# Kernel tuning notes

Hardware: AMD Instinct MI355X
Metric: run time of the kernel (lower is better)

## Reference

```python
import jax, jax.numpy as jnp
import numpy as np

N = 50000      # nodes
E = 625000     # directed edges
F_IN, H1, H2, OUT = 128, 128, 64, 50


def setup_inputs() -> dict:
    key = jax.random.key(0)
    ks = jax.random.split(key, 5)
    x = jax.random.normal(ks[0], (N, F_IN), dtype=jnp.float32)
    edge_index = jax.random.randint(ks[1], (2, E), 0, N, dtype=jnp.int64)
    W1 = jax.random.normal(ks[2], (F_IN, H1), dtype=jnp.float32) * 0.05
    b1 = jnp.zeros((H1,), jnp.float32)
    W2 = jax.random.normal(ks[3], (H1, H2), dtype=jnp.float32) * 0.05
    b2 = jnp.zeros((H2,), jnp.float32)
    Wh = jax.random.normal(ks[4], (H2, OUT), dtype=jnp.float32) * 0.05
    bh = jnp.zeros((OUT,), jnp.float32)
    return {"x": x, "edge_index": edge_index, "W1": W1, "b1": b1,
            "W2": W2, "b2": b2, "Wh": Wh, "bh": bh}


def _gcn_conv(h, W, b, src, dst, dinv, n):
    # h' = D^{-1/2} A_hat D^{-1/2} (h W) + b, A_hat includes self-loops
    h = h @ W                                   # [n, out]
    coef = (dinv[src] * dinv[dst])[:, None]      # [e, 1]
    agg = jax.ops.segment_sum(h[src] * coef, dst, num_segments=n)
    return agg + b


def reference(x, edge_index, W1, b1, W2, b2, Wh, bh):
    n = x.shape[0]
    loops = jnp.arange(n, dtype=edge_index.dtype)
    src = jnp.concatenate([edge_index[0], loops])
    dst = jnp.concatenate([edge_index[1], loops])
    # symmetric GCN normalization: deg over destinations (incl. self-loops)
    deg = jax.ops.segment_sum(jnp.ones(src.shape[0], x.dtype), dst, num_segments=n)
    dinv = jnp.where(deg > 0, jax.lax.rsqrt(deg), 0.0)
    # dropout is a no-op in eval mode (training=False)
    h = _gcn_conv(x, W1, b1, src, dst, dinv, n)
    h = jax.nn.relu(h)
    h = _gcn_conv(h, W2, b2, src, dst, dinv, n)
    h = jax.nn.relu(h)
    return h @ Wh + bh
```

## Files before the change

### kernel.cpp

```cpp
#include <hip/hip_runtime.h>

#define F_IN 128
#define HH1 128
#define HH2 64
#define FOUT 50
#define EB 256
#define NBUCK_MAX 256

typedef __attribute__((ext_vector_type(8))) short short8;
typedef __attribute__((ext_vector_type(4))) short s16x4;
typedef __attribute__((ext_vector_type(4))) float f32x4;

__device__ inline short f2bf(float f) {
    union { float f; unsigned u; } v; v.f = f;
    unsigned r = v.u + 0x7fffu + ((v.u >> 16) & 1u);
    return (short)(r >> 16);
}
__device__ inline float bf2f(short s) {
    union { float f; unsigned u; } v; v.u = ((unsigned)(unsigned short)s) << 16;
    return v.f;
}

__device__ inline int detect64(const unsigned* raw) {
    __shared__ int s_is64;
    if (threadIdx.x == 0) s_is64 = 1;
    __syncthreads();
    if (raw[2 * threadIdx.x + 1] != 0u) atomicAnd(&s_is64, 0);
    __syncthreads();
    return s_is64;
}

__global__ __launch_bounds__(256) void bucket_count(
    const int* __restrict__ raw, int E, int nbuck, int* __restrict__ parthist,
    const float* __restrict__ W1, const float* __restrict__ W2,
    const float* __restrict__ Wh, short* __restrict__ W1t,
    short* __restrict__ W2t, short* __restrict__ Wht) {
    __shared__ int hist[4][NBUCK_MAX];
    const int tid = threadIdx.x;
    const int wv = tid >> 6;
    int is64 = detect64((const unsigned*)raw);
    for (int k = tid; k < 4 * NBUCK_MAX; k += 256) ((int*)hist)[k] = 0;
    __syncthreads();
    const int CH = (E + EB - 1) / EB;
    const int e0 = blockIdx.x * CH, e1 = min(E, e0 + CH);
    for (int e = e0 + tid; e < e1; e += 256) {
        int d = is64 ? raw[2 * (long)E + 2 * e] : raw[E + e];
        atomicAdd(&hist[wv][d >> 8], 1);
    }
    __syncthreads();
    for (int k = tid; k < nbuck; k += 256)
        parthist[blockIdx.x * nbuck + k] =
            hist[0][k] + hist[1][k] + hist[2][k] + hist[3][k];
    const int T1 = HH1 * F_IN, T2 = HH2 * HH1, T3 = 64 * HH2;
    int idx = blockIdx.x * 256 + tid;
    if (idx < T1) {
        int c = idx / F_IN, k = idx - c * F_IN;
        W1t[idx] = f2bf(W1[(long)k * HH1 + c]);
    } else if (idx < T1 + T2) {
        int i = idx - T1;
        int c = i / HH1, k = i - c * HH1;
        W2t[i] = f2bf(W2[(long)k * HH2 + c]);
    } else if (idx < T1 + T2 + T3) {
        int i = idx - T1 - T2;
        int c = i / HH2, k = i - c * HH2;
        Wht[i] = f2bf((c < FOUT) ? Wh[(long)k * FOUT + c] : 0.f);
    }
}

__global__ __launch_bounds__(256) void scan_cols(
    int* __restrict__ parthist, int* __restrict__ totals, int* __restrict__ bbase,
    unsigned* __restrict__ done, int nbuck, int E) {
    const int k = blockIdx.x;
    const int t = threadIdx.x;
    __shared__ int sh[256];
    int v = 0;
    if (k < nbuck) v = parthist[t * nbuck + k];
    sh[t] = v;
    __syncthreads();
    for (int off = 1; off < 256; off <<= 1) {
        int tv = (t >= off) ? sh[t - off] : 0;
        __syncthreads();
        sh[t] += tv;
        __syncthreads();
    }
    if (k < nbuck) parthist[t * nbuck + k] = sh[t] - v;
    if (t == 255) totals[k] = (k < nbuck) ? sh[255] : 0;
    __threadfence();
    __syncthreads();
    __shared__ unsigned s_old;
    if (t == 0) s_old = atomicAdd(done, 1u);
    __syncthreads();
    if (s_old % 256u != 255u) return;
    __threadfence();
    int tv2 = totals[t];
    sh[t] = tv2;
    __syncthreads();
    for (int off = 1; off < 256; off <<= 1) {
        int tt = (t >= off) ? sh[t - off] : 0;
        __syncthreads();
        sh[t] += tt;
        __syncthreads();
    }
    if (t < nbuck) bbase[t] = sh[t] - tv2;
    if (t == 0) bbase[nbuck] = E;
}

__global__ __launch_bounds__(256) void scatter_gemm1(
    const int* __restrict__ raw, int E, int nbuck,
    const int* __restrict__ parthist, const int* __restrict__ bbase,
    int2* __restrict__ tmp,
    const float* __restrict__ x, const short* __restrict__ W1t,
    short* __restrict__ h1, int n) {
    const int tid = threadIdx.x;
    if (blockIdx.x < EB) {
        __shared__ int cur[NBUCK_MAX];
        int is64 = detect64((const unsigned*)raw);
        for (int k = tid; k < nbuck; k += 256)
            cur[k] = bbase[k] + parthist[blockIdx.x * nbuck + k];
        __syncthreads();
        const int CH = (E + EB - 1) / EB;
        const int e0 = blockIdx.x * CH, e1 = min(E, e0 + CH);
        for (int e = e0 + tid; e < e1; e += 256) {
            int s, d;
            if (is64) {
                s = raw[2 * e];
                d = raw[2 * (long)E + 2 * e];
            } else {
                s = raw[e];
                d = raw[E + e];
            }
            int pos = atomicAdd(&cur[d >> 8], 1);
            tmp[pos] = make_int2(s, d);
        }
        return;
    }
    const int bid = blockIdx.x - EB;
    const int wave = tid >> 6;
    const int lane = tid & 63;
    const int l15 = lane & 15;
    const int kg = lane >> 4;
    const int rowbase = bid * 64 + wave * 16;
    const int arow = rowbase + l15;
    constexpr int KS = F_IN / 32;

    short8 af[KS];
    if (arow < n) {
        const float* xr = x + (long)arow * F_IN + kg * 8;
#pragma unroll
        for (int ks = 0; ks < KS; ++ks) {
            float4 f0 = *(const float4*)(xr + ks * 32);
            float4 f1 = *(const float4*)(xr + ks * 32 + 4);
            short8 a;
            a[0] = f2bf(f0.x); a[1] = f2bf(f0.y); a[2] = f2bf(f0.z); a[3] = f2bf(f0.w);
            a[4] = f2bf(f1.x); a[5] = f2bf(f1.y); a[6] = f2bf(f1.z); a[7] = f2bf(f1.w);
            af[ks] = a;
        }
    } else {
#pragma unroll
        for (int ks = 0; ks < KS; ++ks) af[ks] = (short8)0;
    }
    const int crowb = rowbase + kg * 4;
#pragma unroll
    for (int ct = 0; ct < HH1 / 16; ++ct) {
        const int col = ct * 16 + l15;
        const short* wr = W1t + (long)col * F_IN + kg * 8;
        f32x4 acc = {0.f, 0.f, 0.f, 0.f};
#pragma unroll
        for (int ks = 0; ks < KS; ++ks) {
            short8 bfr = *(const short8*)(wr + ks * 32);
            acc = __builtin_amdgcn_mfma_f32_16x16x32_bf16(af[ks], bfr, acc, 0, 0, 0);
        }
#pragma unroll
        for (int j = 0; j < 4; ++j) {
            int r = crowb + j;
            if (r < n) h1[(long)r * HH1 + col] = f2bf(acc[j]);
        }
    }
}

__global__ __launch_bounds__(256) void bucket_finalize(
    const int2* __restrict__ tmp, const int* __restrict__ bbase,
    int* __restrict__ rowptr, float* __restrict__ dinv,
    int* __restrict__ csr_src, int n, int nbuck) {
    __shared__ int deg[256];
    __shared__ int cur[256];
    __shared__ int sh[256];
    const int k = blockIdx.x;
    const int tid = threadIdx.x;
    const int b0 = bbase[k], b1 = bbase[k + 1];
    deg[tid] = 0;
    __syncthreads();
    for (int e = b0 + tid; e < b1; e += 256) atomicAdd(&deg[tmp[e].y & 255], 1);
    __syncthreads();
    int v = deg[tid];
    sh[tid] = v;
    __syncthreads();
    for (int off = 1; off < 256; off <<= 1) {
        int t = (tid >= off) ? sh[tid - off] : 0;
        __syncthreads();
        sh[tid] += t;
        __syncthreads();
    }
    int excl = sh[tid] - v;
    cur[tid] = excl;
    int node = (k << 8) + tid;
    if (node < n) {
        rowptr[node] = b0 + excl;
        dinv[node] = rsqrtf((float)v + 1.0f);
    }
    if (k == 0 && tid == 0) rowptr[n] = bbase[nbuck];
    __syncthreads();
    for (int e = b0 + tid; e < b1; e += 256) {
        int2 sd = tmp[e];
        int p = atomicAdd(&cur[sd.y & 255], 1);
        csr_src[b0 + p] = sd.x;
    }
}

template <int FPL>
__device__ inline void gather1(const short* p0, float c0, float* acc) {
    if constexpr (FPL == 8) {
        short8 v0 = *(const short8*)p0;
#pragma unroll
        for (int j = 0; j < 8; ++j) acc[j] = fmaf(c0, bf2f(v0[j]), acc[j]);
    } else {
        s16x4 v0 = *(const s16x4*)p0;
#pragma unroll
        for (int j = 0; j < 4; ++j) acc[j] = fmaf(c0, bf2f(v0[j]), acc[j]);
    }
}

template <int FW, bool OUT_F32>
__global__ __launch_bounds__(256) void agg_mm(
    const short* __restrict__ h, const int* __restrict__ rowptr,
    const int* __restrict__ csr_src, const float* __restrict__ dinv,
    const float* __restrict__ bias_pre, const short* __restrict__ Wt,
    const float* __restrict__ bias_post, void* __restrict__ Yv, int n,
    int ncreal) {
    constexpr int FPL = FW / 16;
    constexpr int LDW = FW + 8;
    constexpr int KS = FW / 32;
    __shared__ short tile[16][LDW];
    const int tid = threadIdx.x;
    const int grp = tid >> 4;
    const int l16 = tid & 15;
    const int node = blockIdx.x * 16 + grp;

    float acc[FPL];
#pragma unroll
    for (int j = 0; j < FPL; ++j) acc[j] = 0.f;

    if (node < n) {
        const float di = dinv[node];
#pragma unroll
        for (int j = 0; j < FPL; ++j) acc[j] = bias_pre[l16 * FPL + j];
        gather1<FPL>(h + (long)node * FW + l16 * FPL, di * di, acc);
        int e = rowptr[node];
        const int end = rowptr[node + 1];
        for (; e + 3 < end; e += 4) {
            int s0 = csr_src[e];
            int s1 = csr_src[e + 1];
            int s2 = csr_src[e + 2];
            int s3 = csr_src[e + 3];
            const short* p0 = h + (long)s0 * FW + l16 * FPL;
            const short* p1 = h + (long)s1 * FW + l16 * FPL;
            const short* p2 = h + (long)s2 * FW + l16 * FPL;
            const short* p3 = h + (long)s3 * FW + l16 * FPL;
            float c0 = dinv[s0] * di;
            float c1 = dinv[s1] * di;
            float c2 = dinv[s2] * di;
            float c3 = dinv[s3] * di;
            if constexpr (FPL == 8) {
                short8 v0 = *(const short8*)p0;
                short8 v1 = *(const short8*)p1;
                short8 v2 = *(const short8*)p2;
                short8 v3 = *(const short8*)p3;
#pragma unroll
                for (int j = 0; j < 8; ++j) acc[j] = fmaf(c0, bf2f(v0[j]), acc[j]);
#pragma unroll
                for (int j = 0; j < 8; ++j) acc[j] = fmaf(c1, bf2f(v1[j]), acc[j]);
#pragma unroll
                for (int j = 0; j < 8; ++j) acc[j] = fmaf(c2, bf2f(v2[j]), acc[j]);
#pragma unroll
                for (int j = 0; j < 8; ++j) acc[j] = fmaf(c3, bf2f(v3[j]), acc[j]);
            } else {
                s16x4 v0 = *(const s16x4*)p0;
                s16x4 v1 = *(const s16x4*)p1;
                s16x4 v2 = *(const s16x4*)p2;
                s16x4 v3 = *(const s16x4*)p3;
#pragma unroll
                for (int j = 0; j < 4; ++j) acc[j] = fmaf(c0, bf2f(v0[j]), acc[j]);
#pragma unroll
                for (int j = 0; j < 4; ++j) acc[j] = fmaf(c1, bf2f(v1[j]), acc[j]);
#pragma unroll
                for (int j = 0; j < 4; ++j) acc[j] = fmaf(c2, bf2f(v2[j]), acc[j]);
#pragma unroll
                for (int j = 0; j < 4; ++j) acc[j] = fmaf(c3, bf2f(v3[j]), acc[j]);
            }
        }
        for (; e < end; ++e) {
            int s0 = csr_src[e];
            gather1<FPL>(h + (long)s0 * FW + l16 * FPL, dinv[s0] * di, acc);
        }
    }
    if constexpr (FPL == 8) {
        short8 o;
#pragma unroll
        for (int j = 0; j < 8; ++j) o[j] = f2bf(fmaxf(acc[j], 0.f));
        *(short8*)&tile[grp][l16 * 8] = o;
    } else {
        s16x4 o;
#pragma unroll
        for (int j = 0; j < 4; ++j) o[j] = f2bf(fmaxf(acc[j], 0.f));
        *(s16x4*)&tile[grp][l16 * 4] = o;
    }
    __syncthreads();

    const int wave = tid >> 6;
    const int lane = tid & 63;
    const int l15 = lane & 15;
    const int kg = lane >> 4;
    const int col = wave * 16 + l15;
    short8 af[KS];
#pragma unroll
    for (int ks = 0; ks < KS; ++ks)
        af[ks] = *(const short8*)&tile[l15][kg * 8 + ks * 32];
    f32x4 c2 = {0.f, 0.f, 0.f, 0.f};
    const short* wr = Wt + (long)col * FW + kg * 8;
#pragma unroll
    for (int ks = 0; ks < KS; ++ks) {
        short8 bfr = *(const short8*)(wr + ks * 32);
        c2 = __builtin_amdgcn_mfma_f32_16x16x32_bf16(af[ks], bfr, c2, 0, 0, 0);
    }
    const int rb = blockIdx.x * 16 + kg * 4;
    if (OUT_F32) {
        float* Y = (float*)Yv;
#pragma unroll
        for (int j = 0; j < 4; ++j) {
            int g = rb + j;
            if (g < n && col < ncreal)
                Y[(long)g * ncreal + col] = c2[j] + bias_post[col];
        }
    } else {
        short* Y = (short*)Yv;
#pragma unroll
        for (int j = 0; j < 4; ++j) {
            int g = rb + j;
            if (g < n) Y[(long)g * 64 + col] = f2bf(c2[j]);
        }
    }
}

static inline size_t al256(size_t x) { return (x + 255) & ~(size_t)255; }

extern "C" void kernel_launch(void* const* d_in, const int* in_sizes, int n_in,
                              void* d_out, int out_size, void* d_ws, size_t ws_size,
                              hipStream_t stream) {
    const float* x    = (const float*)d_in[0];
    const int*   eraw = (const int*)d_in[1];
    const float* W1   = (const float*)d_in[2];
    const float* b1   = (const float*)d_in[3];
    const float* W2   = (const float*)d_in[4];
    const float* b2   = (const float*)d_in[5];
    const float* Wh   = (const float*)d_in[6];
    const float* bh   = (const float*)d_in[7];
    float* out = (float*)d_out;
    const int n = in_sizes[0] / F_IN;
    const int E = in_sizes[1] / 2;
    const int nbuck = (n + 255) >> 8;

    char* p = (char*)d_ws;
    unsigned* done  = (unsigned*)p; p += 256;
    float* dinv     = (float*)p; p += al256((size_t)n * 4);
    int*   rowptr   = (int*)p;   p += al256((size_t)(n + 1) * 4);
    int*   parthist = (int*)p;   p += al256((size_t)EB * nbuck * 4);
    int*   totals   = (int*)p;   p += al256((size_t)NBUCK_MAX * 4);
    int*   bbase    = (int*)p;   p += al256((size_t)(nbuck + 1) * 4);
    int*   csr_src  = (int*)p;   p += al256((size_t)E * 4);
    short* W1t      = (short*)p; p += al256((size_t)HH1 * F_IN * 2);
    short* W2t      = (short*)p; p += al256((size_t)HH2 * HH1 * 2);
    short* Whtp     = (short*)p; p += al256((size_t)64 * HH2 * 2);
    int2*  tmp      = (int2*)p;  p += al256((size_t)E * 8);
    short* h1       = (short*)p; p += al256((size_t)n * HH1 * 2);
    short* h2       = (short*)p;

    dim3 blk(256);
    bucket_count<<<EB, blk, 0, stream>>>(eraw, E, nbuck, parthist,
                                         W1, W2, Wh, W1t, W2t, Whtp);
    scan_cols<<<NBUCK_MAX, blk, 0, stream>>>(parthist, totals, bbase, done, nbuck, E);
    scatter_gemm1<<<EB + (n + 63) / 64, blk, 0, stream>>>(
        eraw, E, nbuck, parthist, bbase, tmp, x, W1t, h1, n);
    bucket_finalize<<<nbuck, blk, 0, stream>>>(tmp, bbase, rowptr, dinv, csr_src, n, nbuck);

    agg_mm<HH1, false><<<(n + 15) / 16, blk, 0, stream>>>(
        h1, rowptr, csr_src, dinv, b1, W2t, nullptr, h2, n, HH2);
    agg_mm<HH2, true><<<(n + 15) / 16, blk, 0, stream>>>(
        h2, rowptr, csr_src, dinv, b2, Whtp, bh, out, n, FOUT);
}
```

Before: 122.9 us.

## Sort nodes by in-degree within buckets to balance aggregation block work

Measured after the change: 130.7 us. 1.06x slower.

```diff
diff --git a/kernel.cpp b/kernel.cpp
--- a/kernel.cpp
+++ b/kernel.cpp
@@ -181,10 +181,12 @@
 __global__ __launch_bounds__(256) void bucket_finalize(
     const int2* __restrict__ tmp, const int* __restrict__ bbase,
     int* __restrict__ rowptr, float* __restrict__ dinv,
-    int* __restrict__ csr_src, int n, int nbuck) {
+    int* __restrict__ csr_src, int* __restrict__ perm, int n, int nbuck) {
     __shared__ int deg[256];
     __shared__ int cur[256];
     __shared__ int sh[256];
+    __shared__ int dhist[64];
+    __shared__ int dsc[64];
     const int k = blockIdx.x;
     const int tid = threadIdx.x;
     const int b0 = bbase[k], b1 = bbase[k + 1];
@@ -204,7 +206,8 @@
     int excl = sh[tid] - v;
     cur[tid] = excl;
     int node = (k << 8) + tid;
-    if (node < n) {
+    bool valid = (node < n);
+    if (valid) {
         rowptr[node] = b0 + excl;
         dinv[node] = rsqrtf((float)v + 1.0f);
     }
@@ -214,6 +217,25 @@
         int2 sd = tmp[e];
         int p = atomicAdd(&cur[sd.y & 255], 1);
         csr_src[b0 + p] = sd.x;
+    }
+    if (tid < 64) dhist[tid] = 0;
+    __syncthreads();
+    int bin = min(v, 63);
+    if (valid) atomicAdd(&dhist[bin], 1);
+    __syncthreads();
+    if (tid < 64) dsc[tid] = dhist[tid];
+    __syncthreads();
+    for (int off = 1; off < 64; off <<= 1) {
+        int t = (tid < 64 && tid >= off) ? dsc[tid - off] : 0;
+        __syncthreads();
+        if (tid < 64) dsc[tid] += t;
+        __syncthreads();
+    }
+    if (tid < 64) dhist[tid] = dsc[tid] - dhist[tid];
+    __syncthreads();
+    if (valid) {
+        int pos = atomicAdd(&dhist[bin], 1);
+        perm[(k << 8) + pos] = node;
     }
 }
 
@@ -235,22 +257,25 @@
     const short* __restrict__ h, const int* __restrict__ rowptr,
     const int* __restrict__ csr_src, const float* __restrict__ dinv,
     const float* __restrict__ bias_pre, const short* __restrict__ Wt,
-    const float* __restrict__ bias_post, void* __restrict__ Yv, int n,
-    int ncreal) {
+    const float* __restrict__ bias_post, const int* __restrict__ perm,
+    void* __restrict__ Yv, int n, int ncreal) {
     constexpr int FPL = FW / 16;
     constexpr int LDW = FW + 8;
     constexpr int KS = FW / 32;
     __shared__ short tile[16][LDW];
+    __shared__ int s_nodes[16];
     const int tid = threadIdx.x;
     const int grp = tid >> 4;
     const int l16 = tid & 15;
-    const int node = blockIdx.x * 16 + grp;
+    const int idx16 = blockIdx.x * 16 + grp;
+    const int node = (idx16 < n) ? perm[idx16] : -1;
+    if (l16 == 0) s_nodes[grp] = node;
 
     float acc[FPL];
 #pragma unroll
     for (int j = 0; j < FPL; ++j) acc[j] = 0.f;
 
-    if (node < n) {
+    if (node >= 0) {
         const float di = dinv[node];
 #pragma unroll
         for (int j = 0; j < FPL; ++j) acc[j] = bias_pre[l16 * FPL + j];
@@ -332,21 +357,20 @@
         short8 bfr = *(const short8*)(wr + ks * 32);
         c2 = __builtin_amdgcn_mfma_f32_16x16x32_bf16(af[ks], bfr, c2, 0, 0, 0);
     }
-    const int rb = blockIdx.x * 16 + kg * 4;
     if (OUT_F32) {
         float* Y = (float*)Yv;
 #pragma unroll
         for (int j = 0; j < 4; ++j) {
-            int g = rb + j;
-            if (g < n && col < ncreal)
-                Y[(long)g * ncreal + col] = c2[j] + bias_post[col];
+            int gnode = s_nodes[kg * 4 + j];
+            if (gnode >= 0 && col < ncreal)
+                Y[(long)gnode * ncreal + col] = c2[j] + bias_post[col];
         }
     } else {
         short* Y = (short*)Yv;
 #pragma unroll
         for (int j = 0; j < 4; ++j) {
-            int g = rb + j;
-            if (g < n) Y[(long)g * 64 + col] = f2bf(c2[j]);
+            int gnode = s_nodes[kg * 4 + j];
+            if (gnode >= 0) Y[(long)gnode * 64 + col] = f2bf(c2[j]);
         }
     }
 }
@@ -377,6 +401,7 @@
     int*   totals   = (int*)p;   p += al256((size_t)NBUCK_MAX * 4);
     int*   bbase    = (int*)p;   p += al256((size_t)(nbuck + 1) * 4);
     int*   csr_src  = (int*)p;   p += al256((size_t)E * 4);
+    int*   perm     = (int*)p;   p += al256((size_t)n * 4);
     short* W1t      = (short*)p; p += al256((size_t)HH1 * F_IN * 2);
     short* W2t      = (short*)p; p += al256((size_t)HH2 * HH1 * 2);
     short* Whtp     = (short*)p; p += al256((size_t)64 * HH2 * 2);
@@ -390,10 +415,11 @@
     scan_cols<<<NBUCK_MAX, blk, 0, stream>>>(parthist, totals, bbase, done, nbuck, E);
     scatter_gemm1<<<EB + (n + 63) / 64, blk, 0, stream>>>(
         eraw, E, nbuck, parthist, bbase, tmp, x, W1t, h1, n);
-    bucket_finalize<<<nbuck, blk, 0, stream>>>(tmp, bbase, rowptr, dinv, csr_src, n, nbuck);
+    bucket_finalize<<<nbuck, blk, 0, stream>>>(tmp, bbase, rowptr, dinv, csr_src,
+                                               perm, n, nbuck);
 
     agg_mm<HH1, false><<<(n + 15) / 16, blk, 0, stream>>>(
-        h1, rowptr, csr_src, dinv, b1, W2t, nullptr, h2, n, HH2);
+        h1, rowptr, csr_src, dinv, b1, W2t, nullptr, perm, h2, n, HH2);
     agg_mm<HH2, true><<<(n + 15) / 16, blk, 0, stream>>>(
-        h2, rowptr, csr_src, dinv, b2, Whtp, bh, out, n, FOUT);
-}
+        h2, rowptr, csr_src, dinv, b2, Whtp, bh, perm, out, n, FOUT);
+}
```

## Assign one wavefront per node in aggregation instead of 16-lane groups

Applied to the files above, without the earlier changes.

Result: slower. 180.9 us (+47.1%).

```diff
diff --git a/kernel.cpp b/kernel.cpp
--- a/kernel.cpp
+++ b/kernel.cpp
@@ -217,19 +217,6 @@
     }
 }
 
-template <int FPL>
-__device__ inline void gather1(const short* p0, float c0, float* acc) {
-    if constexpr (FPL == 8) {
-        short8 v0 = *(const short8*)p0;
-#pragma unroll
-        for (int j = 0; j < 8; ++j) acc[j] = fmaf(c0, bf2f(v0[j]), acc[j]);
-    } else {
-        s16x4 v0 = *(const s16x4*)p0;
-#pragma unroll
-        for (int j = 0; j < 4; ++j) acc[j] = fmaf(c0, bf2f(v0[j]), acc[j]);
-    }
-}
-
 template <int FW, bool OUT_F32>
 __global__ __launch_bounds__(256) void agg_mm(
     const short* __restrict__ h, const int* __restrict__ rowptr,
@@ -237,24 +224,37 @@
     const float* __restrict__ bias_pre, const short* __restrict__ Wt,
     const float* __restrict__ bias_post, void* __restrict__ Yv, int n,
     int ncreal) {
-    constexpr int FPL = FW / 16;
+    constexpr int SPL = FW / 64;
     constexpr int LDW = FW + 8;
     constexpr int KS = FW / 32;
     __shared__ short tile[16][LDW];
     const int tid = threadIdx.x;
-    const int grp = tid >> 4;
-    const int l16 = tid & 15;
-    const int node = blockIdx.x * 16 + grp;
-
-    float acc[FPL];
-#pragma unroll
-    for (int j = 0; j < FPL; ++j) acc[j] = 0.f;
+    const int wave = tid >> 6;
+    const int lane = tid & 63;
+    const int node = blockIdx.x * 4 + wave;
+
+    for (int i = tid; i < 12 * LDW; i += 256)
+        tile[4 + i / LDW][i - (i / LDW) * LDW] = 0;
+
+    float acc[SPL];
+#pragma unroll
+    for (int j = 0; j < SPL; ++j) acc[j] = 0.f;
 
     if (node < n) {
         const float di = dinv[node];
 #pragma unroll
-        for (int j = 0; j < FPL; ++j) acc[j] = bias_pre[l16 * FPL + j];
-        gather1<FPL>(h + (long)node * FW + l16 * FPL, di * di, acc);
+        for (int j = 0; j < SPL; ++j) acc[j] = bias_pre[lane * SPL + j];
+        {
+            const short* p = h + (long)node * FW + lane * SPL;
+            float c = di * di;
+            if constexpr (SPL == 2) {
+                int v = *(const int*)p;
+                acc[0] = fmaf(c, bf2f((short)(v & 0xffff)), acc[0]);
+                acc[1] = fmaf(c, bf2f((short)(v >> 16)), acc[1]);
+            } else {
+                acc[0] = fmaf(c, bf2f(*p), acc[0]);
+            }
+        }
         int e = rowptr[node];
         const int end = rowptr[node + 1];
         for (; e + 3 < end; e += 4) {
@@ -262,62 +262,61 @@
             int s1 = csr_src[e + 1];
             int s2 = csr_src[e + 2];
             int s3 = csr_src[e + 3];
-            const short* p0 = h + (long)s0 * FW + l16 * FPL;
-            const short* p1 = h + (long)s1 * FW + l16 * FPL;
-            const short* p2 = h + (long)s2 * FW + l16 * FPL;
-            const short* p3 = h + (long)s3 * FW + l16 * FPL;
+            const short* p0 = h + (long)s0 * FW + lane * SPL;
+            const short* p1 = h + (long)s1 * FW + lane * SPL;
+            const short* p2 = h + (long)s2 * FW + lane * SPL;
+            const short* p3 = h + (long)s3 * FW + lane * SPL;
             float c0 = dinv[s0] * di;
             float c1 = dinv[s1] * di;
             float c2 = dinv[s2] * di;
             float c3 = dinv[s3] * di;
-            if constexpr (FPL == 8) {
-                short8 v0 = *(const short8*)p0;
-                short8 v1 = *(const short8*)p1;
-                short8 v2 = *(const short8*)p2;
-                short8 v3 = *(const short8*)p3;
-#pragma unroll
-                for (int j = 0; j < 8; ++j) acc[j] = fmaf(c0, bf2f(v0[j]), acc[j]);
-#pragma unroll
-                for (int j = 0; j < 8; ++j) acc[j] = fmaf(c1, bf2f(v1[j]), acc[j]);
-#pragma unroll
-                for (int j = 0; j < 8; ++j) acc[j] = fmaf(c2, bf2f(v2[j]), acc[j]);
-#pragma unroll
-                for (int j = 0; j < 8; ++j) acc[j] = fmaf(c3, bf2f(v3[j]), acc[j]);
+            if constexpr (SPL == 2) {
+                int v0 = *(const int*)p0;
+                int v1 = *(const int*)p1;
+                int v2 = *(const int*)p2;
+                int v3 = *(const int*)p3;
+                acc[0] = fmaf(c0, bf2f((short)(v0 & 0xffff)), acc[0]);
+                acc[1] = fmaf(c0, bf2f((short)(v0 >> 16)), acc[1]);
+                acc[0] = fmaf(c1, bf2f((short)(v1 & 0xffff)), acc[0]);
+                acc[1] = fmaf(c1, bf2f((short)(v1 >> 16)), acc[1]);
+                acc[0] = fmaf(c2, bf2f((short)(v2 & 0xffff)), acc[0]);
+                acc[1] = fmaf(c2, bf2f((short)(v2 >> 16)), acc[1]);
+                acc[0] = fmaf(c3, bf2f((short)(v3 & 0xffff)), acc[0]);
+                acc[1] = fmaf(c3, bf2f((short)(v3 >> 16)), acc[1]);
             } else {
-                s16x4 v0 = *(const s16x4*)p0;
-                s16x4 v1 = *(const s16x4*)p1;
-                s16x4 v2 = *(const s16x4*)p2;
-                s16x4 v3 = *(const s16x4*)p3;
-#pragma unroll
-                for (int j = 0; j < 4; ++j) acc[j] = fmaf(c0, bf2f(v0[j]), acc[j]);
-#pragma unroll
-                for (int j = 0; j < 4; ++j) acc[j] = fmaf(c1, bf2f(v1[j]), acc[j]);
-#pragma unroll
-                for (int j = 0; j < 4; ++j) acc[j] = fmaf(c2, bf2f(v2[j]), acc[j]);
-#pragma unroll
-                for (int j = 0; j < 4; ++j) acc[j] = fmaf(c3, bf2f(v3[j]), acc[j]);
+                short v0 = *p0;
+                short v1 = *p1;
+                short v2 = *p2;
+                short v3 = *p3;
+                acc[0] = fmaf(c0, bf2f(v0), acc[0]);
+                acc[0] = fmaf(c1, bf2f(v1), acc[0]);
+                acc[0] = fmaf(c2, bf2f(v2), acc[0]);
+                acc[0] = fmaf(c3, bf2f(v3), acc[0]);
             }
         }
         for (; e < end; ++e) {
             int s0 = csr_src[e];
-            gather1<FPL>(h + (long)s0 * FW + l16 * FPL, dinv[s0] * di, acc);
-        }
-    }
-    if constexpr (FPL == 8) {
-        short8 o;
-#pragma unroll
-        for (int j = 0; j < 8; ++j) o[j] = f2bf(fmaxf(acc[j], 0.f));
-        *(short8*)&tile[grp][l16 * 8] = o;
+            const short* p = h + (long)s0 * FW + lane * SPL;
+            float c = dinv[s0] * di;
+            if constexpr (SPL == 2) {
+                int v = *(const int*)p;
+                acc[0] = fmaf(c, bf2f((short)(v & 0xffff)), acc[0]);
+                acc[1] = fmaf(c, bf2f((short)(v >> 16)), acc[1]);
+            } else {
+                acc[0] = fmaf(c, bf2f(*p), acc[0]);
+            }
+        }
+    }
+    if constexpr (SPL == 2) {
+        short o0 = f2bf(fmaxf(acc[0], 0.f));
+        short o1 = f2bf(fmaxf(acc[1], 0.f));
+        *(int*)&tile[wave][lane * 2] =
+            ((int)(unsigned short)o1 << 16) | (unsigned short)o0;
     } else {
-        s16x4 o;
-#pragma unroll
-        for (int j = 0; j < 4; ++j) o[j] = f2bf(fmaxf(acc[j], 0.f));
-        *(s16x4*)&tile[grp][l16 * 4] = o;
-    }
-    __syncthreads();
-
-    const int wave = tid >> 6;
-    const int lane = tid & 63;
+        tile[wave][lane] = f2bf(fmaxf(acc[0], 0.f));
+    }
+    __syncthreads();
+
     const int l15 = lane & 15;
     const int kg = lane >> 4;
     const int col = wave * 16 + l15;
@@ -332,21 +331,22 @@
         short8 bfr = *(const short8*)(wr + ks * 32);
         c2 = __builtin_amdgcn_mfma_f32_16x16x32_bf16(af[ks], bfr, c2, 0, 0, 0);
     }
-    const int rb = blockIdx.x * 16 + kg * 4;
     if (OUT_F32) {
         float* Y = (float*)Yv;
 #pragma unroll
         for (int j = 0; j < 4; ++j) {
-            int g = rb + j;
-            if (g < n && col < ncreal)
+            int r = kg * 4 + j;
+            int g = blockIdx.x * 4 + r;
+            if (r < 4 && g < n && col < ncreal)
                 Y[(long)g * ncreal + col] = c2[j] + bias_post[col];
         }
     } else {
         short* Y = (short*)Yv;
 #pragma unroll
         for (int j = 0; j < 4; ++j) {
-            int g = rb + j;
-            if (g < n) Y[(long)g * 64 + col] = f2bf(c2[j]);
+            int r = kg * 4 + j;
+            int g = blockIdx.x * 4 + r;
+            if (r < 4 && g < n) Y[(long)g * 64 + col] = f2bf(c2[j]);
         }
     }
 }
@@ -392,8 +392,8 @@
         eraw, E, nbuck, parthist, bbase, tmp, x, W1t, h1, n);
     bucket_finalize<<<nbuck, blk, 0, stream>>>(tmp, bbase, rowptr, dinv, csr_src, n, nbuck);
 
-    agg_mm<HH1, false><<<(n + 15) / 16, blk, 0, stream>>>(
+    agg_mm<HH1, false><<<(n + 3) / 4, blk, 0, stream>>>(
         h1, rowptr, csr_src, dinv, b1, W2t, nullptr, h2, n, HH2);
-    agg_mm<HH2, true><<<(n + 15) / 16, blk, 0, stream>>>(
+    agg_mm<HH2, true><<<(n + 3) / 4, blk, 0, stream>>>(
         h2, rowptr, csr_src, dinv, b2, Whtp, bh, out, n, FOUT);
 }
```
